# Performance work log

Measured on AMD Instinct MI355X. Metric: run time of the kernel, lower is better.

The kernel has to match this reference:

```python
import jax, jax.numpy as jnp
import numpy as np

DIM = 512
NUM_HEADS = 8
HEAD_DIM = DIM // NUM_HEADS
SCALE = HEAD_DIM ** -0.5


def setup_inputs() -> dict:
    key = jax.random.key(0)
    ks = jax.random.split(key, 5)
    B, N = 4, 2048
    x = jax.random.normal(ks[0], (B, N, DIM), dtype=jnp.float32)
    # Learned parameters (torch nn.Linear style: y = x @ W.T + b)
    w_qkv = jax.random.normal(ks[1], (3 * DIM, DIM), dtype=jnp.float32) * (DIM ** -0.5)
    b_qkv = jnp.zeros((3 * DIM,), dtype=jnp.float32)
    w_proj = jax.random.normal(ks[2], (DIM, DIM), dtype=jnp.float32) * (DIM ** -0.5)
    b_proj = jnp.zeros((DIM,), dtype=jnp.float32)
    return {"x": x, "w_qkv": w_qkv, "b_qkv": b_qkv, "w_proj": w_proj, "b_proj": b_proj}


def reference(x, w_qkv, b_qkv, w_proj, b_proj):
    B, N, C = x.shape
    qkv = x @ w_qkv.T + b_qkv                      # [B, N, 3C]
    qkv = qkv.reshape(B, N, 3, NUM_HEADS, HEAD_DIM)
    qkv = jnp.transpose(qkv, (2, 0, 3, 1, 4))      # [3, B, H, N, d]
    q, k, v = qkv[0], qkv[1], qkv[2]
    attn = jnp.einsum("bhqd,bhkd->bhqk", q, k) * SCALE  # [B, H, N, N]
    attn = jax.nn.softmax(attn, axis=-1)
    out = jnp.einsum("bhqk,bhkd->bhqd", attn, v)   # [B, H, N, d]
    out = jnp.transpose(out, (0, 2, 1, 3)).reshape(B, N, C)
    return out @ w_proj.T + b_proj
```

## Files before the change

kernel.cpp:

```cpp
#include <hip/hip_runtime.h>

#define DIM 512
#define NHEAD 8
#define HDIM 64
#define BATCH 4
#define SEQ 2048
#define MTOT (BATCH*SEQ)
#define SCALE 0.125f
#define LOG2E 1.4426950408889634f

typedef __bf16 bf16_t;
typedef __bf16 bf16x8 __attribute__((ext_vector_type(8)));
typedef __bf16 bf16x4 __attribute__((ext_vector_type(4)));
typedef float f32x4 __attribute__((ext_vector_type(4)));

#define ASYNC_COPY16(g, l) __builtin_amdgcn_global_load_lds( \
    (const __attribute__((address_space(1))) void*)(g),      \
    (__attribute__((address_space(3))) void*)(l), 16, 0, 0)

#define NX_ELEM  (4194304)
#define NWQ_ELEM (786432)
#define NWP_ELEM (262144)
__global__ __launch_bounds__(256) void cvt_kernel(const float* __restrict__ x,
                                                  const float* __restrict__ wq,
                                                  const float* __restrict__ wp,
                                                  bf16_t* __restrict__ out) {
    int i = (blockIdx.x * 256 + threadIdx.x) * 4;
    const float* src;
    if (i < NX_ELEM)                 src = x  + i;
    else if (i < NX_ELEM + NWQ_ELEM) src = wq + (i - NX_ELEM);
    else                             src = wp + (i - NX_ELEM - NWQ_ELEM);
    float4 v = *reinterpret_cast<const float4*>(src);
    bf16x4 o;
    o[0] = (bf16_t)v.x; o[1] = (bf16_t)v.y; o[2] = (bf16_t)v.z; o[3] = (bf16_t)v.w;
    *reinterpret_cast<bf16x4*>(out + i) = o;
}

__global__ __launch_bounds__(256) void gemm_qkv_kernel(
    const bf16_t* __restrict__ X, const bf16_t* __restrict__ W,
    const float* __restrict__ bias,
    bf16_t* __restrict__ Qo, bf16_t* __restrict__ Ko, bf16_t* __restrict__ Vto)
{
    __shared__ bf16_t As[2][128][64];
    __shared__ bf16_t Bs[2][128][64];
    const int tid = threadIdx.x;
    const int wave = tid >> 6, lane = tid & 63;
    const int lhi = lane >> 4, llo = lane & 15;
    const int o = blockIdx.x;
    const int x = o & 7, i0 = o >> 3;
    const int m0 = (x * 8 + (i0 & 7)) * 128;
    const int n0 = (i0 >> 3) * 128;
    const int wr = (wave >> 1) * 64, wc = (wave & 1) * 64;
    f32x4 acc[4][4] = {};

    const int srow = wave * 32 + (lane >> 3);
    const int scol = (lane & 7) * 8;
    const bf16_t* gA = X + (size_t)(m0 + srow) * DIM + scol;
    const bf16_t* gB = W + (size_t)(n0 + srow) * DIM + scol;

    #pragma unroll
    for (int p = 0; p < 4; ++p) {
        ASYNC_COPY16(gA + (size_t)p * 8 * DIM, &As[0][wave*32 + p*8][0]);
        ASYNC_COPY16(gB + (size_t)p * 8 * DIM, &Bs[0][wave*32 + p*8][0]);
    }
    __syncthreads();

    for (int ki = 0; ki < 8; ++ki) {
        const int cur = ki & 1, nxt = cur ^ 1;
        if (ki + 1 < 8) {
            const int k0n = (ki + 1) * 64;
            #pragma unroll
            for (int p = 0; p < 4; ++p) {
                ASYNC_COPY16(gA + (size_t)p * 8 * DIM + k0n, &As[nxt][wave*32 + p*8][0]);
                ASYNC_COPY16(gB + (size_t)p * 8 * DIM + k0n, &Bs[nxt][wave*32 + p*8][0]);
            }
        }
        #pragma unroll
        for (int ks = 0; ks < 2; ++ks) {
            bf16x8 af[4], bfr[4];
            #pragma unroll
            for (int i = 0; i < 4; ++i)
                af[i] = *reinterpret_cast<const bf16x8*>(&As[cur][wr + i*16 + llo][ks*32 + lhi*8]);
            #pragma unroll
            for (int j = 0; j < 4; ++j)
                bfr[j] = *reinterpret_cast<const bf16x8*>(&Bs[cur][wc + j*16 + llo][ks*32 + lhi*8]);
            __builtin_amdgcn_s_setprio(1);
            #pragma unroll
            for (int i = 0; i < 4; ++i)
                #pragma unroll
                for (int j = 0; j < 4; ++j)
                    acc[i][j] = __builtin_amdgcn_mfma_f32_16x16x32_bf16(af[i], bfr[j], acc[i][j], 0, 0, 0);
            __builtin_amdgcn_s_setprio(0);
        }
        __syncthreads();
    }

    #pragma unroll
    for (int j = 0; j < 4; ++j) {
        int col = n0 + wc + j*16 + llo;
        int which = col >> 9;
        int hh = (col >> 6) & 7;
        int dd = col & 63;
        float bv = bias[col];
        #pragma unroll
        for (int i = 0; i < 4; ++i) {
            #pragma unroll
            for (int r = 0; r < 4; ++r) {
                int m = m0 + wr + i*16 + lhi*4 + r;
                int b = m >> 11, ns = m & 2047;
                float v = acc[i][j][r] + bv;
                size_t bh = (size_t)(b * NHEAD + hh);
                if (which == 0)
                    Qo[(bh * SEQ + ns) * HDIM + dd] = (bf16_t)(v * (SCALE * LOG2E));
                else if (which == 1)
                    Ko[(bh * SEQ + ns) * HDIM + dd] = (bf16_t)v;
                else
                    Vto[(bh * HDIM + dd) * SEQ + ns] = (bf16_t)v;
            }
        }
    }
}

__global__ __launch_bounds__(512) void attn_kernel(
    const bf16_t* __restrict__ Q, const bf16_t* __restrict__ K,
    const bf16_t* __restrict__ Vt, bf16_t* __restrict__ O)
{
    __shared__ bf16_t Ks[2][64][64];
    __shared__ bf16_t Vs[2][64][64];
    const int tid = threadIdx.x;
    const int wave = tid >> 6, lane = tid & 63;
    const int lhi = lane >> 4, llo = lane & 15;
    const int o = blockIdx.x;
    const int w = (o & 7) * 32 + (o >> 3);
    const int qt = w & 7, bh = w >> 3;
    const bf16_t* Qb = Q + (size_t)bh * SEQ * HDIM;
    const bf16_t* Kb = K + (size_t)bh * SEQ * HDIM;
    const bf16_t* Vb = Vt + (size_t)bh * HDIM * SEQ;
    const int q0 = qt * 256 + wave * 32;

    const int ksr = tid >> 3, kg = tid & 7;
    const int kcol = (kg * 8) ^ ((ksr & 7) * 8);
    const int vd = tid >> 3, vg = tid & 7;
    const int pkA = (32*(vg>>2) + 8*((2*vg)&3)   + 4*((vg>>1)&1)) ^ ((vd & 7) * 8);
    const int pkB = (32*(vg>>2) + 8*((2*vg+1)&3) + 4*((vg>>1)&1)) ^ ((vd & 7) * 8);

    bf16x8 aq[2][2];
    #pragma unroll
    for (int qb = 0; qb < 2; ++qb)
        #pragma unroll
        for (int ks = 0; ks < 2; ++ks)
            aq[qb][ks] = *reinterpret_cast<const bf16x8*>(
                Qb + (size_t)(q0 + qb*16 + llo) * HDIM + ks*32 + lhi*8);

    f32x4 acc_o[2][4] = {};
    float mstat[2], lstat[2];
    lstat[0] = lstat[1] = 0.f;
    const float THR = 8.0f * LOG2E;
    const int NT = SEQ / 64;

    uint4 kreg, vreg;

    bf16x8 apA[2][2], apB[2][2];
    bf16x8 bvA[2][4], bvB[2][4];

    kreg = *reinterpret_cast<const uint4*>(Kb + (size_t)ksr * HDIM + kg*8);
    vreg = *reinterpret_cast<const uint4*>(Vb + (size_t)vd * SEQ + vg*8);
    *reinterpret_cast<uint4*>(&Ks[0][ksr][kcol]) = kreg;
    *reinterpret_cast<uint2*>(&Vs[0][vd][pkA]) = make_uint2(vreg.x, vreg.y);
    *reinterpret_cast<uint2*>(&Vs[0][vd][pkB]) = make_uint2(vreg.z, vreg.w);
    __syncthreads();

    kreg = *reinterpret_cast<const uint4*>(Kb + (size_t)(64 + ksr) * HDIM + kg*8);
    vreg = *reinterpret_cast<const uint4*>(Vb + (size_t)vd * SEQ + 64 + vg*8);

    {
        f32x4 s[2][4] = {};
        __builtin_amdgcn_s_setprio(1);
        #pragma unroll
        for (int kb = 0; kb < 4; ++kb)
            #pragma unroll
            for (int ks = 0; ks < 2; ++ks) {
                bf16x8 kf = *reinterpret_cast<const bf16x8*>(
                    &Ks[0][kb*16 + llo][(ks*32 + lhi*8) ^ ((llo & 7) * 8)]);
                #pragma unroll
                for (int qb = 0; qb < 2; ++qb)
                    s[qb][kb] = __builtin_amdgcn_mfma_f32_16x16x32_bf16(kf, aq[qb][ks], s[qb][kb], 0, 0, 0);
            }
        __builtin_amdgcn_s_setprio(0);
        #pragma unroll
        for (int qb = 0; qb < 2; ++qb) {
            float mx = s[qb][0][0];
            #pragma unroll
            for (int kb = 0; kb < 4; ++kb)
                #pragma unroll
                for (int r = 0; r < 4; ++r) mx = fmaxf(mx, s[qb][kb][r]);
            mx = fmaxf(mx, __shfl_xor(mx, 16, 64));
            mx = fmaxf(mx, __shfl_xor(mx, 32, 64));
            mstat[qb] = mx;
            float rs = 0.f;
            #pragma unroll
            for (int kp = 0; kp < 2; ++kp)
                #pragma unroll
                for (int j = 0; j < 4; ++j) {
                    float p0 = __builtin_amdgcn_exp2f(s[qb][2*kp][j]     - mx);
                    float p1 = __builtin_amdgcn_exp2f(s[qb][2*kp + 1][j] - mx);
                    rs += p0 + p1;
                    apA[qb][kp][j]     = (bf16_t)p0;
                    apA[qb][kp][4 + j] = (bf16_t)p1;
                }
            lstat[qb] = rs;
        }
        #pragma unroll
        for (int kp = 0; kp < 2; ++kp)
            #pragma unroll
            for (int db = 0; db < 4; ++db)
                bvA[kp][db] = *reinterpret_cast<const bf16x8*>(
                    &Vs[0][db*16 + llo][(kp*32 + lhi*8) ^ ((llo & 7) * 8)]);
        *reinterpret_cast<uint4*>(&Ks[1][ksr][kcol]) = kreg;
        *reinterpret_cast<uint2*>(&Vs[1][vd][pkA]) = make_uint2(vreg.x, vreg.y);
        *reinterpret_cast<uint2*>(&Vs[1][vd][pkB]) = make_uint2(vreg.z, vreg.w);
        __syncthreads();
    }

    auto body = [&](int kt, bf16x8 (&apIn)[2][2], bf16x8 (&bvIn)[2][4],
                    bf16x8 (&apOut)[2][2], bf16x8 (&bvOut)[2][4]) {
        const int cur = kt & 1, nxt = cur ^ 1;
        if (kt + 1 < NT) {
            const size_t koff = (size_t)(kt + 1) * 64;
            kreg = *reinterpret_cast<const uint4*>(Kb + (koff + ksr) * HDIM + kg*8);
            vreg = *reinterpret_cast<const uint4*>(Vb + (size_t)vd * SEQ + koff + vg*8);
        }
        f32x4 s[2][4] = {};
        __builtin_amdgcn_s_setprio(1);
        #pragma unroll
        for (int kb = 0; kb < 4; ++kb)
            #pragma unroll
            for (int ks = 0; ks < 2; ++ks) {
                bf16x8 kf = *reinterpret_cast<const bf16x8*>(
                    &Ks[cur][kb*16 + llo][(ks*32 + lhi*8) ^ ((llo & 7) * 8)]);
                #pragma unroll
                for (int qb = 0; qb < 2; ++qb)
                    s[qb][kb] = __builtin_amdgcn_mfma_f32_16x16x32_bf16(kf, aq[qb][ks], s[qb][kb], 0, 0, 0);
            }
        __builtin_amdgcn_s_setprio(0);

        float lmax[2];
        bool ok = true;
        #pragma unroll
        for (int qb = 0; qb < 2; ++qb) {
            float mx = s[qb][0][0];
            #pragma unroll
            for (int kb = 0; kb < 4; ++kb)
                #pragma unroll
                for (int r = 0; r < 4; ++r) mx = fmaxf(mx, s[qb][kb][r]);
            lmax[qb] = mx;
            ok &= (mx <= mstat[qb] + THR);
        }
        if (!__all(ok)) {
            #pragma unroll
            for (int kp = 0; kp < 2; ++kp)
                #pragma unroll
                for (int db = 0; db < 4; ++db)
                    #pragma unroll
                    for (int qb = 0; qb < 2; ++qb)
                        acc_o[qb][db] = __builtin_amdgcn_mfma_f32_16x16x32_bf16(apIn[qb][kp], bvIn[kp][db], acc_o[qb][db], 0, 0, 0);
            #pragma unroll
            for (int kp = 0; kp < 2; ++kp)
                #pragma unroll
                for (int db = 0; db < 4; ++db)
                    #pragma unroll
                    for (int e = 0; e < 8; ++e) bvIn[kp][db][e] = (bf16_t)0.f;
            #pragma unroll
            for (int qb = 0; qb < 2; ++qb) {
                float mx = lmax[qb];
                mx = fmaxf(mx, __shfl_xor(mx, 16, 64));
                mx = fmaxf(mx, __shfl_xor(mx, 32, 64));
                float mold = mstat[qb];
                float mn = fmaxf(mold, mx);
                float alpha = __builtin_amdgcn_exp2f(mold - mn);
                mstat[qb] = mn;
                lstat[qb] *= alpha;
                #pragma unroll
                for (int r = 0; r < 4; ++r) {
                    float av = __shfl(alpha, (lane & 48) >> 2 | r, 64);
                    #pragma unroll
                    for (int db = 0; db < 4; ++db) acc_o[qb][db][r] *= av;
                }
            }
        }

        __builtin_amdgcn_s_setprio(1);
        #pragma unroll
        for (int kp = 0; kp < 2; ++kp) {
            #pragma unroll
            for (int qb = 0; qb < 2; ++qb) {
                float rs = 0.f;
                #pragma unroll
                for (int j = 0; j < 4; ++j) {
                    float p0 = __builtin_amdgcn_exp2f(s[qb][2*kp][j]     - mstat[qb]);
                    float p1 = __builtin_amdgcn_exp2f(s[qb][2*kp + 1][j] - mstat[qb]);
                    rs += p0 + p1;
                    apOut[qb][kp][j]     = (bf16_t)p0;
                    apOut[qb][kp][4 + j] = (bf16_t)p1;
                }
                lstat[qb] += rs;
            }
            #pragma unroll
            for (int db = 0; db < 4; ++db)
                #pragma unroll
                for (int qb = 0; qb < 2; ++qb)
                    acc_o[qb][db] = __builtin_amdgcn_mfma_f32_16x16x32_bf16(apIn[qb][kp], bvIn[kp][db], acc_o[qb][db], 0, 0, 0);
        }
        __builtin_amdgcn_s_setprio(0);

        #pragma unroll
        for (int kp = 0; kp < 2; ++kp)
            #pragma unroll
            for (int db = 0; db < 4; ++db)
                bvOut[kp][db] = *reinterpret_cast<const bf16x8*>(
                    &Vs[cur][db*16 + llo][(kp*32 + lhi*8) ^ ((llo & 7) * 8)]);

        if (kt + 1 < NT) {
            *reinterpret_cast<uint4*>(&Ks[nxt][ksr][kcol]) = kreg;
            *reinterpret_cast<uint2*>(&Vs[nxt][vd][pkA]) = make_uint2(vreg.x, vreg.y);
            *reinterpret_cast<uint2*>(&Vs[nxt][vd][pkB]) = make_uint2(vreg.z, vreg.w);
        }
        __syncthreads();
    };

    for (int tp = 1; tp + 1 < NT; tp += 2) {
        body(tp,     apA, bvA, apB, bvB);
        body(tp + 1, apB, bvB, apA, bvA);
    }
    body(NT - 1, apA, bvA, apB, bvB);

    #pragma unroll
    for (int kp = 0; kp < 2; ++kp)
        #pragma unroll
        for (int db = 0; db < 4; ++db)
            #pragma unroll
            for (int qb = 0; qb < 2; ++qb)
                acc_o[qb][db] = __builtin_amdgcn_mfma_f32_16x16x32_bf16(apB[qb][kp], bvB[kp][db], acc_o[qb][db], 0, 0, 0);

    const int b = bh >> 3, h = bh & 7;
    #pragma unroll
    for (int qb = 0; qb < 2; ++qb) {
        float r = lstat[qb];
        r += __shfl_xor(r, 16, 64);
        r += __shfl_xor(r, 32, 64);
        lstat[qb] = r;
    }
    #pragma unroll
    for (int qb = 0; qb < 2; ++qb) {
        float inv = 1.0f / lstat[qb];
        #pragma unroll
        for (int r = 0; r < 4; ++r) {
            float iv = __shfl(inv, (lane & 48) >> 2 | r, 64);
            int q = q0 + qb*16 + lhi*4 + r;
            #pragma unroll
            for (int db = 0; db < 4; ++db)
                O[(size_t)(b * SEQ + q) * DIM + h*HDIM + db*16 + llo] =
                    (bf16_t)(acc_o[qb][db][r] * iv);
        }
    }
}

__global__ __launch_bounds__(256) void gemm_proj_kernel(
    const bf16_t* __restrict__ X, const bf16_t* __restrict__ W,
    const float* __restrict__ bias, float* __restrict__ out)
{
    __shared__ bf16_t As[2][128][64];
    __shared__ bf16_t Bs[2][128][64];
    const int tid = threadIdx.x;
    const int wave = tid >> 6, lane = tid & 63;
    const int lhi = lane >> 4, llo = lane & 15;
    const int o = blockIdx.x;
    const int x = o & 7, i0 = o >> 3;
    const int m0 = (x * 8 + (i0 & 7)) * 128;
    const int n0 = (i0 >> 3) * 128;
    const int wr = (wave >> 1) * 64, wc = (wave & 1) * 64;
    f32x4 acc[4][4] = {};

    const int srow = wave * 32 + (lane >> 3);
    const int scol = (lane & 7) * 8;
    const bf16_t* gA = X + (size_t)(m0 + srow) * DIM + scol;
    const bf16_t* gB = W + (size_t)(n0 + srow) * DIM + scol;

    #pragma unroll
    for (int p = 0; p < 4; ++p) {
        ASYNC_COPY16(gA + (size_t)p * 8 * DIM, &As[0][wave*32 + p*8][0]);
        ASYNC_COPY16(gB + (size_t)p * 8 * DIM, &Bs[0][wave*32 + p*8][0]);
    }
    __syncthreads();

    for (int ki = 0; ki < 8; ++ki) {
        const int cur = ki & 1, nxt = cur ^ 1;
        if (ki + 1 < 8) {
            const int k0n = (ki + 1) * 64;
            #pragma unroll
            for (int p = 0; p < 4; ++p) {
                ASYNC_COPY16(gA + (size_t)p * 8 * DIM + k0n, &As[nxt][wave*32 + p*8][0]);
                ASYNC_COPY16(gB + (size_t)p * 8 * DIM + k0n, &Bs[nxt][wave*32 + p*8][0]);
            }
        }
        #pragma unroll
        for (int ks = 0; ks < 2; ++ks) {
            bf16x8 af[4], bfr[4];
            #pragma unroll
            for (int i = 0; i < 4; ++i)
                af[i] = *reinterpret_cast<const bf16x8*>(&As[cur][wr + i*16 + llo][ks*32 + lhi*8]);
            #pragma unroll
            for (int j = 0; j < 4; ++j)
                bfr[j] = *reinterpret_cast<const bf16x8*>(&Bs[cur][wc + j*16 + llo][ks*32 + lhi*8]);
            __builtin_amdgcn_s_setprio(1);
            #pragma unroll
            for (int i = 0; i < 4; ++i)
                #pragma unroll
                for (int j = 0; j < 4; ++j)
                    acc[i][j] = __builtin_amdgcn_mfma_f32_16x16x32_bf16(af[i], bfr[j], acc[i][j], 0, 0, 0);
            __builtin_amdgcn_s_setprio(0);
        }
        __syncthreads();
    }

    #pragma unroll
    for (int j = 0; j < 4; ++j) {
        int col = n0 + wc + j*16 + llo;
        float bv = bias[col];
        #pragma unroll
        for (int i = 0; i < 4; ++i)
            #pragma unroll
            for (int r = 0; r < 4; ++r) {
                int m = m0 + wr + i*16 + lhi*4 + r;
                out[(size_t)m * DIM + col] = acc[i][j][r] + bv;
            }
    }
}

extern "C" void kernel_launch(void* const* d_in, const int* in_sizes, int n_in,
                              void* d_out, int out_size, void* d_ws, size_t ws_size,
                              hipStream_t stream) {
    const float* x      = (const float*)d_in[0];
    const float* w_qkv  = (const float*)d_in[1];
    const float* b_qkv  = (const float*)d_in[2];
    const float* w_proj = (const float*)d_in[3];
    const float* b_proj = (const float*)d_in[4];
    float* out = (float*)d_out;

    const size_t NX  = (size_t)MTOT * DIM;
    const size_t NWQ = (size_t)3 * DIM * DIM;
    const size_t NWP = (size_t)DIM * DIM;
    const size_t NQ  = (size_t)BATCH * NHEAD * SEQ * HDIM;

    bf16_t* Xb    = (bf16_t*)d_ws;
    bf16_t* Wqkv  = Xb + NX;
    bf16_t* Wproj = Wqkv + NWQ;
    bf16_t* Qb    = Wproj + NWP;
    bf16_t* Kb    = Qb + NQ;
    bf16_t* Vtb   = Kb + NQ;
    bf16_t* AOb   = Vtb + NQ;

    cvt_kernel<<<(int)((NX + NWQ + NWP) / 1024), 256, 0, stream>>>(x, w_qkv, w_proj, Xb);

    gemm_qkv_kernel<<<768, 256, 0, stream>>>(Xb, Wqkv, b_qkv, Qb, Kb, Vtb);

    attn_kernel<<<256, 512, 0, stream>>>(Qb, Kb, Vtb, AOb);

    gemm_proj_kernel<<<256, 256, 0, stream>>>(AOb, Wproj, b_proj, out);
}
```

Baseline: 95.45 us.

## Stage V-transpose through LDS, single-buffer GEMMs, halve proj tile width

In the QKV GEMM, the V output tile is first written into shared memory with an XOR swizzle and then stored to the transposed V buffer as coalesced 16-byte rows. Before, each bf16 was scattered with a stride of SEQ. Both GEMMs drop double-buffered async loads for a single buffer with a sync per K step, which reduces LDS use but exposes load latency. The projection GEMM switches to 128x64 tiles over 512 blocks to raise occupancy and fill more CUs. The cvt offset expression is rewritten but evaluates to the same value.

```diff
diff --git a/kernel.cpp b/kernel.cpp
--- a/kernel.cpp
+++ b/kernel.cpp
@@ -12,6 +12,7 @@
 typedef __bf16 bf16_t;
 typedef __bf16 bf16x8 __attribute__((ext_vector_type(8)));
 typedef __bf16 bf16x4 __attribute__((ext_vector_type(4)));
+typedef __bf16 bf16x2 __attribute__((ext_vector_type(2)));
 typedef float f32x4 __attribute__((ext_vector_type(4)));
 
 #define ASYNC_COPY16(g, l) __builtin_amdgcn_global_load_lds( \
@@ -29,7 +30,7 @@
     const float* src;
     if (i < NX_ELEM)                 src = x  + i;
     else if (i < NX_ELEM + NWQ_ELEM) src = wq + (i - NX_ELEM);
-    else                             src = wp + (i - NX_ELEM - NWQ_ELEM);
+    else                             src = wp + (i - NX_ELEM - NWP_ELEM - NWQ_ELEM + NWP_ELEM);
     float4 v = *reinterpret_cast<const float4*>(src);
     bf16x4 o;
     o[0] = (bf16_t)v.x; o[1] = (bf16_t)v.y; o[2] = (bf16_t)v.z; o[3] = (bf16_t)v.w;
@@ -41,8 +42,10 @@
     const float* __restrict__ bias,
     bf16_t* __restrict__ Qo, bf16_t* __restrict__ Ko, bf16_t* __restrict__ Vto)
 {
-    __shared__ bf16_t As[2][128][64];
-    __shared__ bf16_t Bs[2][128][64];
+    __shared__ bf16_t smem[16384];
+    bf16_t (*As)[64] = reinterpret_cast<bf16_t (*)[64]>(smem);
+    bf16_t (*Bs)[64] = reinterpret_cast<bf16_t (*)[64]>(smem + 8192);
+    unsigned int* Lw = reinterpret_cast<unsigned int*>(smem);
     const int tid = threadIdx.x;
     const int wave = tid >> 6, lane = tid & 63;
     const int lhi = lane >> 4, llo = lane & 15;
@@ -58,32 +61,22 @@
     const bf16_t* gA = X + (size_t)(m0 + srow) * DIM + scol;
     const bf16_t* gB = W + (size_t)(n0 + srow) * DIM + scol;
 
-    #pragma unroll
-    for (int p = 0; p < 4; ++p) {
-        ASYNC_COPY16(gA + (size_t)p * 8 * DIM, &As[0][wave*32 + p*8][0]);
-        ASYNC_COPY16(gB + (size_t)p * 8 * DIM, &Bs[0][wave*32 + p*8][0]);
-    }
-    __syncthreads();
-
-    for (int ki = 0; ki < 8; ++ki) {
-        const int cur = ki & 1, nxt = cur ^ 1;
-        if (ki + 1 < 8) {
-            const int k0n = (ki + 1) * 64;
-            #pragma unroll
-            for (int p = 0; p < 4; ++p) {
-                ASYNC_COPY16(gA + (size_t)p * 8 * DIM + k0n, &As[nxt][wave*32 + p*8][0]);
-                ASYNC_COPY16(gB + (size_t)p * 8 * DIM + k0n, &Bs[nxt][wave*32 + p*8][0]);
-            }
-        }
+    for (int k0 = 0; k0 < DIM; k0 += 64) {
+        #pragma unroll
+        for (int p = 0; p < 4; ++p) {
+            ASYNC_COPY16(gA + (size_t)p * 8 * DIM + k0, &As[wave*32 + p*8][0]);
+            ASYNC_COPY16(gB + (size_t)p * 8 * DIM + k0, &Bs[wave*32 + p*8][0]);
+        }
+        __syncthreads();
         #pragma unroll
         for (int ks = 0; ks < 2; ++ks) {
             bf16x8 af[4], bfr[4];
             #pragma unroll
             for (int i = 0; i < 4; ++i)
-                af[i] = *reinterpret_cast<const bf16x8*>(&As[cur][wr + i*16 + llo][ks*32 + lhi*8]);
+                af[i] = *reinterpret_cast<const bf16x8*>(&As[wr + i*16 + llo][ks*32 + lhi*8]);
             #pragma unroll
             for (int j = 0; j < 4; ++j)
-                bfr[j] = *reinterpret_cast<const bf16x8*>(&Bs[cur][wc + j*16 + llo][ks*32 + lhi*8]);
+                bfr[j] = *reinterpret_cast<const bf16x8*>(&Bs[wc + j*16 + llo][ks*32 + lhi*8]);
             __builtin_amdgcn_s_setprio(1);
             #pragma unroll
             for (int i = 0; i < 4; ++i)
@@ -95,28 +88,60 @@
         __syncthreads();
     }
 
-    #pragma unroll
-    for (int j = 0; j < 4; ++j) {
-        int col = n0 + wc + j*16 + llo;
-        int which = col >> 9;
-        int hh = (col >> 6) & 7;
-        int dd = col & 63;
-        float bv = bias[col];
-        #pragma unroll
-        for (int i = 0; i < 4; ++i) {
-            #pragma unroll
-            for (int r = 0; r < 4; ++r) {
-                int m = m0 + wr + i*16 + lhi*4 + r;
-                int b = m >> 11, ns = m & 2047;
-                float v = acc[i][j][r] + bv;
-                size_t bh = (size_t)(b * NHEAD + hh);
-                if (which == 0)
-                    Qo[(bh * SEQ + ns) * HDIM + dd] = (bf16_t)(v * (SCALE * LOG2E));
-                else if (which == 1)
-                    Ko[(bh * SEQ + ns) * HDIM + dd] = (bf16_t)v;
-                else
-                    Vto[(bh * HDIM + dd) * SEQ + ns] = (bf16_t)v;
-            }
+    const int b = m0 >> 11, ns0 = m0 & 2047;
+
+    if (n0 < 1024) {
+        #pragma unroll
+        for (int j = 0; j < 4; ++j) {
+            int col = n0 + wc + j*16 + llo;
+            int which = col >> 9;
+            int hh = (col >> 6) & 7;
+            int dd = col & 63;
+            float bv = bias[col];
+            size_t bh = (size_t)(b * NHEAD + hh);
+            #pragma unroll
+            for (int i = 0; i < 4; ++i) {
+                #pragma unroll
+                for (int r = 0; r < 4; ++r) {
+                    int ns = ns0 + wr + i*16 + lhi*4 + r;
+                    float v = acc[i][j][r] + bv;
+                    if (which == 0)
+                        Qo[(bh * SEQ + ns) * HDIM + dd] = (bf16_t)(v * (SCALE * LOG2E));
+                    else
+                        Ko[(bh * SEQ + ns) * HDIM + dd] = (bf16_t)v;
+                }
+            }
+        }
+    } else {
+        #pragma unroll
+        for (int j = 0; j < 4; ++j) {
+            int ddc = wc + j*16 + llo;
+            float bv = bias[n0 + ddc];
+            int xsw = (ddc & 7) * 4;
+            #pragma unroll
+            for (int i = 0; i < 4; ++i) {
+                int dwb = (wr >> 1) + i*8 + lhi*2;
+                #pragma unroll
+                for (int r2 = 0; r2 < 2; ++r2) {
+                    bf16x2 t;
+                    t[0] = (bf16_t)(acc[i][j][2*r2]     + bv);
+                    t[1] = (bf16_t)(acc[i][j][2*r2 + 1] + bv);
+                    Lw[ddc * 64 + ((dwb + r2) ^ xsw)] = __builtin_bit_cast(unsigned int, t);
+                }
+            }
+        }
+        __syncthreads();
+        const int hh_base = (n0 - 1024) >> 6;
+        const int chunk = tid & 15;
+        #pragma unroll
+        for (int rd = 0; rd < 8; ++rd) {
+            int ddc = rd * 16 + (tid >> 4);
+            uint4 val = *reinterpret_cast<const uint4*>(
+                &Lw[ddc * 64 + ((chunk * 4) ^ ((ddc & 7) * 4))]);
+            int dd = ddc & 63;
+            int hh = hh_base + (ddc >> 6);
+            size_t bh = (size_t)(b * NHEAD + hh);
+            *reinterpret_cast<uint4*>(Vto + (bh * HDIM + dd) * SEQ + ns0 + chunk * 8) = val;
         }
     }
 }
@@ -159,7 +184,6 @@
     const int NT = SEQ / 64;
 
     uint4 kreg, vreg;
-
     bf16x8 apA[2][2], apB[2][2];
     bf16x8 bvA[2][4], bvB[2][4];
 
@@ -369,54 +393,46 @@
     const bf16_t* __restrict__ X, const bf16_t* __restrict__ W,
     const float* __restrict__ bias, float* __restrict__ out)
 {
-    __shared__ bf16_t As[2][128][64];
-    __shared__ bf16_t Bs[2][128][64];
+    __shared__ bf16_t As[128][64];
+    __shared__ bf16_t Bs[64][64];
     const int tid = threadIdx.x;
     const int wave = tid >> 6, lane = tid & 63;
     const int lhi = lane >> 4, llo = lane & 15;
     const int o = blockIdx.x;
     const int x = o & 7, i0 = o >> 3;
     const int m0 = (x * 8 + (i0 & 7)) * 128;
-    const int n0 = (i0 >> 3) * 128;
-    const int wr = (wave >> 1) * 64, wc = (wave & 1) * 64;
-    f32x4 acc[4][4] = {};
+    const int n0 = (i0 >> 3) * 64;
+    const int wr = (wave >> 1) * 64, wc = (wave & 1) * 32;
+    f32x4 acc[4][2] = {};
 
     const int srow = wave * 32 + (lane >> 3);
+    const int srowB = wave * 16 + (lane >> 3);
     const int scol = (lane & 7) * 8;
     const bf16_t* gA = X + (size_t)(m0 + srow) * DIM + scol;
-    const bf16_t* gB = W + (size_t)(n0 + srow) * DIM + scol;
-
-    #pragma unroll
-    for (int p = 0; p < 4; ++p) {
-        ASYNC_COPY16(gA + (size_t)p * 8 * DIM, &As[0][wave*32 + p*8][0]);
-        ASYNC_COPY16(gB + (size_t)p * 8 * DIM, &Bs[0][wave*32 + p*8][0]);
-    }
-    __syncthreads();
-
-    for (int ki = 0; ki < 8; ++ki) {
-        const int cur = ki & 1, nxt = cur ^ 1;
-        if (ki + 1 < 8) {
-            const int k0n = (ki + 1) * 64;
-            #pragma unroll
-            for (int p = 0; p < 4; ++p) {
-                ASYNC_COPY16(gA + (size_t)p * 8 * DIM + k0n, &As[nxt][wave*32 + p*8][0]);
-                ASYNC_COPY16(gB + (size_t)p * 8 * DIM + k0n, &Bs[nxt][wave*32 + p*8][0]);
-            }
-        }
+    const bf16_t* gB = W + (size_t)(n0 + srowB) * DIM + scol;
+
+    for (int k0 = 0; k0 < DIM; k0 += 64) {
+        #pragma unroll
+        for (int p = 0; p < 4; ++p)
+            ASYNC_COPY16(gA + (size_t)p * 8 * DIM + k0, &As[wave*32 + p*8][0]);
+        #pragma unroll
+        for (int p = 0; p < 2; ++p)
+            ASYNC_COPY16(gB + (size_t)p * 8 * DIM + k0, &Bs[wave*16 + p*8][0]);
+        __syncthreads();
         #pragma unroll
         for (int ks = 0; ks < 2; ++ks) {
-            bf16x8 af[4], bfr[4];
+            bf16x8 af[4], bfr[2];
             #pragma unroll
             for (int i = 0; i < 4; ++i)
-                af[i] = *reinterpret_cast<const bf16x8*>(&As[cur][wr + i*16 + llo][ks*32 + lhi*8]);
-            #pragma unroll
-            for (int j = 0; j < 4; ++j)
-                bfr[j] = *reinterpret_cast<const bf16x8*>(&Bs[cur][wc + j*16 + llo][ks*32 + lhi*8]);
+                af[i] = *reinterpret_cast<const bf16x8*>(&As[wr + i*16 + llo][ks*32 + lhi*8]);
+            #pragma unroll
+            for (int j = 0; j < 2; ++j)
+                bfr[j] = *reinterpret_cast<const bf16x8*>(&Bs[wc + j*16 + llo][ks*32 + lhi*8]);
             __builtin_amdgcn_s_setprio(1);
             #pragma unroll
             for (int i = 0; i < 4; ++i)
                 #pragma unroll
-                for (int j = 0; j < 4; ++j)
+                for (int j = 0; j < 2; ++j)
                     acc[i][j] = __builtin_amdgcn_mfma_f32_16x16x32_bf16(af[i], bfr[j], acc[i][j], 0, 0, 0);
             __builtin_amdgcn_s_setprio(0);
         }
@@ -424,7 +440,7 @@
     }
 
     #pragma unroll
-    for (int j = 0; j < 4; ++j) {
+    for (int j = 0; j < 2; ++j) {
         int col = n0 + wc + j*16 + llo;
         float bv = bias[col];
         #pragma unroll
@@ -466,5 +482,5 @@
 
     attn_kernel<<<256, 512, 0, stream>>>(Qb, Kb, Vtb, AOb);
 
-    gemm_proj_kernel<<<256, 256, 0, stream>>>(AOb, Wproj, b_proj, out);
+    gemm_proj_kernel<<<512, 256, 0, stream>>>(AOb, Wproj, b_proj, out);
 }
```

Result: faster. 90.93 us (-4.7%).
